# Kernel optimization log

Hardware: AMD Instinct MI355X
Metric: run time of the kernel (lower is better)

Reference implementation:

```python
import jax, jax.numpy as jnp
import numpy as np

DIM = 768
NUM_HEADS = 12
HEAD_DIM = DIM // NUM_HEADS
SCALE = HEAD_DIM ** -0.5


def setup_inputs() -> dict:
    key = jax.random.key(0)
    k1, k2, k3, k4, k5 = jax.random.split(key, 5)
    B, N = 8, 2048
    x = jax.random.normal(k1, (B, N, DIM), dtype=jnp.float32)
    mask = jax.random.randint(k2, (B, N), 0, 2, dtype=jnp.int32)
    # ensure at least one valid key per batch row to avoid all -inf softmax rows
    mask = mask.at[:, 0].set(1)
    w_qkv = jax.random.normal(k3, (DIM, 3 * DIM), dtype=jnp.float32) * (DIM ** -0.5)
    w_proj = jax.random.normal(k4, (DIM, DIM), dtype=jnp.float32) * (DIM ** -0.5)
    b_proj = jax.random.normal(k5, (DIM,), dtype=jnp.float32) * 0.02
    return {"x": x, "mask": mask, "w_qkv": w_qkv, "w_proj": w_proj, "b_proj": b_proj}


def reference(x, mask, w_qkv, w_proj, b_proj):
    B, N, C = x.shape
    qkv = (x @ w_qkv).reshape(B, N, 3, NUM_HEADS, HEAD_DIM)
    qkv = jnp.transpose(qkv, (2, 0, 3, 1, 4))  # [3, B, H, N, D]
    q, k, v = qkv[0], qkv[1], qkv[2]
    q = q * SCALE
    # fp32 upcast for scores (inputs already fp32; explicit for fidelity)
    attn = jnp.einsum('bhqd,bhkd->bhqk', q.astype(jnp.float32), k.astype(jnp.float32))
    key_mask = mask.astype(bool)[:, None, None, :]  # [B,1,1,N]
    attn = jnp.where(key_mask, attn, -jnp.inf)
    attn = jax.nn.softmax(attn, axis=-1).astype(x.dtype)
    out = jnp.einsum('bhqk,bhkd->bhqd', attn, v)  # [B,H,N,D]
    out = jnp.transpose(out, (0, 2, 1, 3)).reshape(B, N, C)
    return out @ w_proj + b_proj
```

## Files before the change

kernel.cpp:

```cpp
#include <hip/hip_runtime.h>
#include <hip/hip_bf16.h>
#include <stdint.h>

#define NHEAD 12
#define SEQ   2048
#define NB    8
#define MTOK  (NB*SEQ)
#define DIMC  768
#define QKVN  (3*DIMC)

typedef __attribute__((ext_vector_type(8))) short bf16x8;
typedef __attribute__((ext_vector_type(4))) float f32x4;
typedef __attribute__((ext_vector_type(16))) float f32x16;
typedef __attribute__((ext_vector_type(4))) unsigned short u16x4;
typedef __attribute__((ext_vector_type(4))) unsigned int u32x4;

typedef const __attribute__((address_space(1))) char glb_char;
typedef __attribute__((address_space(3))) char lds_char;

__device__ __forceinline__ unsigned short f2bf(float f) {
  union { float f; unsigned u; } v; v.f = f;
  return (unsigned short)((v.u + 0x7FFFu + ((v.u >> 16) & 1u)) >> 16);
}

__device__ __forceinline__ void gload_lds16(const void* g, void* l) {
  __builtin_amdgcn_global_load_lds((glb_char*)g, (lds_char*)l, 16, 0, 0);
}

__device__ __forceinline__ unsigned cvtpk_bf16(float lo, float hi) {
  unsigned d;
  asm("v_cvt_pk_bf16_f32 %0, %1, %2" : "=v"(d) : "v"(lo), "v"(hi));
  return d;
}

#define QSCALE 0.18033688011112042f
#define MASKBIAS -30000.0f

__global__ void __launch_bounds__(256, 8)
cvt_bf16_kernel(const float* __restrict__ in,
                unsigned short* __restrict__ out, int n4) {
  int idx = blockIdx.x * blockDim.x + threadIdx.x;
  int stride = gridDim.x * blockDim.x;
  for (int i = idx; i < n4; i += stride) {
    float4 v = ((const float4*)in)[i];
    u16x4 o;
    o.x = f2bf(v.x); o.y = f2bf(v.y); o.z = f2bf(v.z); o.w = f2bf(v.w);
    ((u16x4*)out)[i] = o;
  }
}

__global__ void __launch_bounds__(256, 4)
maskscan_kernel(const int* __restrict__ mask, int* __restrict__ posmap,
                float* __restrict__ mbias_c, int* __restrict__ nvalid) {
  __shared__ int sums[256];
  __shared__ int btot;
  const int b = blockIdx.x, t = threadIdx.x;
  const int* m = mask + b * SEQ;
  int loc[8];
  int s = 0;
  #pragma unroll
  for (int i = 0; i < 8; i++) { loc[i] = (m[t * 8 + i] != 0) ? 1 : 0; s += loc[i]; }
  sums[t] = s;
  __syncthreads();
  for (int off = 1; off < 256; off <<= 1) {
    int v = (t >= off) ? sums[t - off] : 0;
    __syncthreads();
    sums[t] += v;
    __syncthreads();
  }
  int excl = sums[t] - s;
  if (t == 255) btot = sums[255];
  __syncthreads();
  const int nv = btot;
  #pragma unroll
  for (int i = 0; i < 8; i++) {
    posmap[b * SEQ + t * 8 + i] = loc[i] ? excl : -1;
    excl += loc[i];
  }
  for (int j = t; j < SEQ; j += 256)
    mbias_c[b * SEQ + j] = (j < nv) ? 0.0f : MASKBIAS;
  if (t == 0) nvalid[b] = nv;
}

__global__ void __launch_bounds__(256, 8)
zerotail_kernel(unsigned short* __restrict__ kc, unsigned short* __restrict__ vc,
                const int* __restrict__ nvalid) {
  const int bh = blockIdx.x, t = threadIdx.x;
  const int b = bh / NHEAD;
  const int nv = nvalid[b];
  const int pad = (nv + 63) & ~63;
  const int nz = pad - nv;
  if (nz == 0) return;
  unsigned short* kcb = kc + (size_t)bh * SEQ * 64;
  unsigned short* vcb = vc + (size_t)bh * 64 * SEQ;
  for (int i = t; i < nz * 64; i += 256) {
    int r = i >> 6, d = i & 63;
    kcb[(nv + r) * 64 + d] = 0;
  }
  for (int i = t; i < 64 * nz; i += 256) {
    int d = i / nz, c = i - d * nz;
    vcb[(size_t)d * SEQ + nv + c] = 0;
  }
}

__global__ void __launch_bounds__(256, 8)
transpose_cvt_kernel(const float* __restrict__ in,
                     unsigned short* __restrict__ out,
                     int R, int C) {
  __shared__ float tile[32][33];
  int c0 = blockIdx.x * 32, r0 = blockIdx.y * 32;
  int tx = threadIdx.x & 31, ty = threadIdx.x >> 5;
  #pragma unroll
  for (int i = 0; i < 32; i += 8)
    tile[ty + i][tx] = in[(size_t)(r0 + ty + i) * C + c0 + tx];
  __syncthreads();
  #pragma unroll
  for (int i = 0; i < 32; i += 8)
    out[(size_t)(c0 + ty + i) * R + r0 + tx] = f2bf(tile[tx][ty + i]);
}

__global__ void __launch_bounds__(256, 2)
qkv_gemm_kernel(const unsigned short* __restrict__ xb,
                const unsigned short* __restrict__ wT,
                unsigned short* __restrict__ qo,
                unsigned short* __restrict__ ko,
                unsigned short* __restrict__ vto,
                const int* __restrict__ posmap) {
  __shared__ short lA[2][128 * 32];
  __shared__ short lB[2][128 * 32];
  const int t = threadIdx.x;
  const int lane = t & 63, w = t >> 6;
  const int m0 = blockIdx.x * 128;
  const int n0 = blockIdx.y * 128;
  const int wr = (w >> 1) * 64, wc = (w & 1) * 64;
  const int l15 = lane & 15, lg = lane >> 4;
  const int sr = t >> 2;
  const int sc = t & 3;

  auto STAGE = [&](int k0, int bsel) {
    #pragma unroll
    for (int i = 0; i < 2; i++) {
      int row = i * 64 + sr;
      int cb = (sc ^ ((row >> 1) & 3)) * 8;
      gload_lds16(xb + (size_t)(m0 + row) * DIMC + k0 + cb,
                  (char*)lA + bsel * 8192 + i * 4096 + w * 1024);
      gload_lds16(wT + (size_t)(n0 + row) * DIMC + k0 + cb,
                  (char*)lB + bsel * 8192 + i * 4096 + w * 1024);
    }
  };

  f32x4 acc[4][4] = {};

  STAGE(0, 0);
  asm volatile("s_waitcnt vmcnt(0)" ::: "memory");
  __builtin_amdgcn_s_barrier();

  for (int k0 = 0; k0 < DIMC; k0 += 32) {
    const int bsel = (k0 >> 5) & 1;
    if (k0 + 32 < DIMC) STAGE(k0 + 32, bsel ^ 1);
    const short* A = &lA[bsel][0];
    const short* B = &lB[bsel][0];

    bf16x8 af[4], bfr[4];
    #pragma unroll
    for (int mi = 0; mi < 4; mi++) {
      int m = wr + mi * 16 + l15;
      af[mi] = *(const bf16x8*)&A[m * 32 + ((lg ^ ((m >> 1) & 3)) << 3)];
    }
    #pragma unroll
    for (int nj = 0; nj < 4; nj++) {
      int n = wc + nj * 16 + l15;
      bfr[nj] = *(const bf16x8*)&B[n * 32 + ((lg ^ ((n >> 1) & 3)) << 3)];
    }
    __builtin_amdgcn_s_setprio(1);
    #pragma unroll
    for (int mi = 0; mi < 4; mi++)
      #pragma unroll
      for (int nj = 0; nj < 4; nj++)
        acc[mi][nj] = __builtin_amdgcn_mfma_f32_16x16x32_bf16(af[mi], bfr[nj], acc[mi][nj], 0, 0, 0);
    __builtin_amdgcn_s_setprio(0);

    if (k0 + 32 < DIMC) {
      asm volatile("s_waitcnt vmcnt(0)" ::: "memory");
      __builtin_amdgcn_s_barrier();
    }
  }

  #pragma unroll
  for (int mi = 0; mi < 4; mi++) {
    int tok0 = m0 + wr + mi * 16 + 4 * lg;
    int bb = tok0 >> 11;
    int nn0 = tok0 & 2047;
    int pm[4];
    #pragma unroll
    for (int r = 0; r < 4; r++) pm[r] = posmap[tok0 + r];
    #pragma unroll
    for (int nj = 0; nj < 4; nj++) {
      int col = n0 + wc + nj * 16 + l15;
      int which = col / DIMC;
      int ch = col - which * DIMC;
      int hh = ch >> 6, dd = ch & 63;
      size_t hb = (size_t)(bb * NHEAD + hh);
      if (which == 0) {
        size_t base = (hb * SEQ + nn0) * 64 + dd;
        #pragma unroll
        for (int r = 0; r < 4; r++)
          qo[base + (size_t)r * 64] = f2bf(acc[mi][nj][r] * QSCALE);
      } else if (which == 1) {
        #pragma unroll
        for (int r = 0; r < 4; r++)
          if (pm[r] >= 0)
            ko[(hb * SEQ + pm[r]) * 64 + dd] = f2bf(acc[mi][nj][r]);
      } else {
        #pragma unroll
        for (int r = 0; r < 4; r++)
          if (pm[r] >= 0)
            vto[(hb * 64 + dd) * SEQ + pm[r]] = f2bf(acc[mi][nj][r]);
      }
    }
  }
}

__global__ void __launch_bounds__(256, 4)
attn_kernel(const unsigned short* __restrict__ qbuf,
            const unsigned short* __restrict__ kbuf,
            const unsigned short* __restrict__ vtbuf,
            const float* __restrict__ mbias_c,
            const int* __restrict__ nvalid,
            unsigned short* __restrict__ ao) {
  __shared__ short lKV[2][8192];
  __shared__ float lmask[2][64];
  const int t = threadIdx.x, lane = t & 63, w = t >> 6;
  const int l31 = lane & 31, hi = lane >> 5;
  const int bid = blockIdx.x;
  const int qt = bid / 96;
  const int bh = bid - qt * 96;
  const int b = bh / NHEAD, h = bh - b * NHEAD;
  const int q0 = qt * 128 + w * 32;
  const unsigned short* qb = qbuf + (size_t)bh * SEQ * 64;
  const unsigned short* kb = kbuf + (size_t)bh * SEQ * 64;
  const unsigned short* vb = vtbuf + (size_t)bh * 64 * SEQ;
  const float* mb = mbias_c + b * SEQ;
  const int ntiles = (nvalid[b] + 63) >> 6;

  auto STAGE = [&](int tile, int bsel) {
    int kv0 = tile * 64;
    #pragma unroll
    for (int i = 0; i < 2; i++) {
      int c = i * 4 + w;
      gload_lds16(kb + (size_t)(kv0 + lane) * 64 + c * 8,
                  (char*)lKV + bsel * 16384 + c * 1024);
      gload_lds16(vb + (size_t)lane * SEQ + kv0 + c * 8,
                  (char*)lKV + bsel * 16384 + 8192 + c * 1024);
    }
    if (w == 0)
      __builtin_amdgcn_global_load_lds((glb_char*)(mb + tile * 64 + lane),
                                       (lds_char*)&lmask[bsel][0], 4, 0, 0);
  };

  bf16x8 qf[4];
  #pragma unroll
  for (int dblk = 0; dblk < 4; dblk++)
    qf[dblk] = *(const bf16x8*)(qb + (size_t)(q0 + l31) * 64 + dblk * 16 + hi * 8);

  f32x16 O[2] = {};
  float ls[4] = {0.f, 0.f, 0.f, 0.f};

  STAGE(0, 0);
  __syncthreads();

  for (int it = 0; it < ntiles; ++it) {
    const int bsel = it & 1;
    const short* Kb = &lKV[bsel][0];
    const short* Vb = &lKV[bsel][4096];
    if (it + 1 < ntiles) STAGE(it + 1, bsel ^ 1);

    #pragma unroll
    for (int kb2 = 0; kb2 < 2; kb2++) {
      f32x4 mb4[4];
      #pragma unroll
      for (int g = 0; g < 4; g++)
        mb4[g] = *(const f32x4*)&lmask[bsel][kb2 * 32 + g * 8 + hi * 4];
      f32x16 S;
      #pragma unroll
      for (int r = 0; r < 16; r++) S[r] = mb4[r >> 2][r & 3];

      __builtin_amdgcn_s_setprio(1);
      #pragma unroll
      for (int dblk = 0; dblk < 4; dblk++) {
        bf16x8 kf = *(const bf16x8*)&Kb[(dblk * 2 + hi) * 512 + (kb2 * 32 + l31) * 8];
        S = __builtin_amdgcn_mfma_f32_32x32x16_bf16(kf, qf[dblk], S, 0, 0, 0);
      }
      __builtin_amdgcn_s_setprio(0);

      float p[16];
      #pragma unroll
      for (int r = 0; r < 16; r++) p[r] = __builtin_amdgcn_exp2f(S[r]);
      #pragma unroll
      for (int r = 0; r < 16; r++) ls[r & 3] += p[r];

      #pragma unroll
      for (int half = 0; half < 2; half++) {
        unsigned a0 = cvtpk_bf16(p[half * 8 + 0], p[half * 8 + 1]);
        unsigned a1 = cvtpk_bf16(p[half * 8 + 2], p[half * 8 + 3]);
        unsigned a2 = cvtpk_bf16(p[half * 8 + 4], p[half * 8 + 5]);
        unsigned a3 = cvtpk_bf16(p[half * 8 + 6], p[half * 8 + 7]);
        asm("v_permlane32_swap_b32 %0, %1" : "+v"(a0), "+v"(a2));
        asm("v_permlane32_swap_b32 %0, %1" : "+v"(a1), "+v"(a3));
        union { u32x4 u; bf16x8 f; } cv;
        cv.u = (u32x4){a0, a1, a2, a3};
        __builtin_amdgcn_s_setprio(1);
        #pragma unroll
        for (int dt = 0; dt < 2; dt++) {
          bf16x8 vf = *(const bf16x8*)&Vb[(kb2 * 4 + half * 2 + hi) * 512 + (dt * 32 + l31) * 8];
          O[dt] = __builtin_amdgcn_mfma_f32_32x32x16_bf16(cv.f, vf, O[dt], 0, 0, 0);
        }
        __builtin_amdgcn_s_setprio(0);
      }
    }

    if (it + 1 < ntiles) {
      asm volatile("s_waitcnt vmcnt(0)" ::: "memory");
      __builtin_amdgcn_s_barrier();
    }
  }

  float* lrs = (float*)&lKV[0][0];
  float tot = (ls[0] + ls[1]) + (ls[2] + ls[3]);
  tot += __shfl_xor(tot, 32);
  lrs[w * 32 + l31] = tot;

  float inv[16];
  #pragma unroll
  for (int r = 0; r < 16; r++)
    inv[r] = 1.0f / lrs[w * 32 + (r & 3) + 8 * (r >> 2) + 4 * hi];

  #pragma unroll
  for (int dt = 0; dt < 2; dt++) {
    #pragma unroll
    for (int r = 0; r < 16; r++) {
      int qrow = q0 + (r & 3) + 8 * (r >> 2) + 4 * hi;
      size_t base = ((size_t)(b * SEQ + qrow)) * DIMC + h * 64 + dt * 32 + l31;
      ao[base] = __bfloat16_as_ushort(__float2bfloat16(O[dt][r] * inv[r]));
    }
  }
}

__global__ void __launch_bounds__(256, 2)
proj_gemm_kernel(const unsigned short* __restrict__ ab,
                 const unsigned short* __restrict__ wT,
                 const float* __restrict__ bias,
                 float* __restrict__ out) {
  __shared__ short lA[2][128 * 32];
  __shared__ short lB[2][128 * 32];
  const int t = threadIdx.x;
  const int lane = t & 63, w = t >> 6;
  const int m0 = blockIdx.x * 128;
  const int n0 = blockIdx.y * 128;
  const int wr = (w >> 1) * 64, wc = (w & 1) * 64;
  const int l15 = lane & 15, lg = lane >> 4;
  const int sr = t >> 2;
  const int sc = t & 3;

  auto STAGE = [&](int k0, int bsel) {
    #pragma unroll
    for (int i = 0; i < 2; i++) {
      int row = i * 64 + sr;
      int cb = (sc ^ ((row >> 1) & 3)) * 8;
      gload_lds16(ab + (size_t)(m0 + row) * DIMC + k0 + cb,
                  (char*)lA + bsel * 8192 + i * 4096 + w * 1024);
      gload_lds16(wT + (size_t)(n0 + row) * DIMC + k0 + cb,
                  (char*)lB + bsel * 8192 + i * 4096 + w * 1024);
    }
  };

  f32x4 acc[4][4] = {};

  STAGE(0, 0);
  asm volatile("s_waitcnt vmcnt(0)" ::: "memory");
  __builtin_amdgcn_s_barrier();

  for (int k0 = 0; k0 < DIMC; k0 += 32) {
    const int bsel = (k0 >> 5) & 1;
    if (k0 + 32 < DIMC) STAGE(k0 + 32, bsel ^ 1);
    const short* A = &lA[bsel][0];
    const short* B = &lB[bsel][0];

    bf16x8 af[4], bfr[4];
    #pragma unroll
    for (int mi = 0; mi < 4; mi++) {
      int m = wr + mi * 16 + l15;
      af[mi] = *(const bf16x8*)&A[m * 32 + ((lg ^ ((m >> 1) & 3)) << 3)];
    }
    #pragma unroll
    for (int nj = 0; nj < 4; nj++) {
      int n = wc + nj * 16 + l15;
      bfr[nj] = *(const bf16x8*)&B[n * 32 + ((lg ^ ((n >> 1) & 3)) << 3)];
    }
    __builtin_amdgcn_s_setprio(1);
    #pragma unroll
    for (int mi = 0; mi < 4; mi++)
      #pragma unroll
      for (int nj = 0; nj < 4; nj++)
        acc[mi][nj] = __builtin_amdgcn_mfma_f32_16x16x32_bf16(af[mi], bfr[nj], acc[mi][nj], 0, 0, 0);
    __builtin_amdgcn_s_setprio(0);

    if (k0 + 32 < DIMC) {
      asm volatile("s_waitcnt vmcnt(0)" ::: "memory");
      __builtin_amdgcn_s_barrier();
    }
  }

  #pragma unroll
  for (int mi = 0; mi < 4; mi++) {
    int row0 = m0 + wr + mi * 16 + 4 * lg;
    #pragma unroll
    for (int nj = 0; nj < 4; nj++) {
      int col = n0 + wc + nj * 16 + l15;
      float bv = bias[col];
      #pragma unroll
      for (int r = 0; r < 4; r++)
        out[(size_t)(row0 + r) * DIMC + col] = acc[mi][nj][r] + bv;
    }
  }
}

extern "C" void kernel_launch(void* const* d_in, const int* in_sizes, int n_in,
                              void* d_out, int out_size, void* d_ws, size_t ws_size,
                              hipStream_t stream) {
  const float* x      = (const float*)d_in[0];
  const int*   mask   = (const int*)d_in[1];
  const float* w_qkv  = (const float*)d_in[2];
  const float* w_proj = (const float*)d_in[3];
  const float* b_proj = (const float*)d_in[4];
  float* out = (float*)d_out;

  unsigned short* ws = (unsigned short*)d_ws;
  unsigned short* xb     = ws;
  unsigned short* wqkvT  = xb    + (size_t)MTOK * DIMC;
  unsigned short* wprojT = wqkvT + (size_t)QKVN * DIMC;
  unsigned short* qbuf   = wprojT + (size_t)DIMC * DIMC;
  unsigned short* kbuf   = qbuf  + (size_t)MTOK * DIMC;
  unsigned short* vtbuf  = kbuf  + (size_t)MTOK * DIMC;
  float*          mbias_c = (float*)(vtbuf + (size_t)MTOK * DIMC);
  int*            posmap  = (int*)(mbias_c + MTOK);
  int*            nvalid  = posmap + MTOK;
  unsigned short* aob    = xb;

  cvt_bf16_kernel<<<2048, 256, 0, stream>>>(x, xb, MTOK * DIMC / 4);
  maskscan_kernel<<<NB, 256, 0, stream>>>(mask, posmap, mbias_c, nvalid);
  transpose_cvt_kernel<<<dim3(QKVN / 32, DIMC / 32), 256, 0, stream>>>(w_qkv, wqkvT, DIMC, QKVN);
  transpose_cvt_kernel<<<dim3(DIMC / 32, DIMC / 32), 256, 0, stream>>>(w_proj, wprojT, DIMC, DIMC);
  qkv_gemm_kernel<<<dim3(128, 18), 256, 0, stream>>>(xb, wqkvT, qbuf, kbuf, vtbuf, posmap);
  zerotail_kernel<<<NB * NHEAD, 256, 0, stream>>>(kbuf, vtbuf, nvalid);
  attn_kernel<<<1536, 256, 0, stream>>>(qbuf, kbuf, vtbuf, mbias_c, nvalid, aob);
  proj_gemm_kernel<<<dim3(128, 6), 256, 0, stream>>>(aob, wprojT, b_proj, out);
}
```

Baseline: 218.9 us.

## Triple-buffer LDS staging in QKV and projection GEMMs with partial vmcnt waits

Both bf16 GEMM kernels move from a double-buffered to a triple-buffered LDS pipeline, loading two K-tiles ahead. Each iteration waits with vmcnt(4) for only the current tile's loads, so the next tile's loads stay in flight, and it uses a single barrier per iteration instead of a full drain. Launch bounds change from 2 to 3 blocks per SM. The intent is to hide global-load latency behind MFMA work, at the cost of more LDS per block and a tighter register budget.

```diff
diff --git a/kernel.cpp b/kernel.cpp
--- a/kernel.cpp
+++ b/kernel.cpp
@@ -119,15 +119,15 @@
     out[(size_t)(c0 + ty + i) * R + r0 + tx] = f2bf(tile[tx][ty + i]);
 }
 
-__global__ void __launch_bounds__(256, 2)
+__global__ void __launch_bounds__(256, 3)
 qkv_gemm_kernel(const unsigned short* __restrict__ xb,
                 const unsigned short* __restrict__ wT,
                 unsigned short* __restrict__ qo,
                 unsigned short* __restrict__ ko,
                 unsigned short* __restrict__ vto,
                 const int* __restrict__ posmap) {
-  __shared__ short lA[2][128 * 32];
-  __shared__ short lB[2][128 * 32];
+  __shared__ short lA[3][128 * 32];
+  __shared__ short lB[3][128 * 32];
   const int t = threadIdx.x;
   const int lane = t & 63, w = t >> 6;
   const int m0 = blockIdx.x * 128;
@@ -150,16 +150,22 @@
   };
 
   f32x4 acc[4][4] = {};
+  const int NT = DIMC / 32;
 
   STAGE(0, 0);
-  asm volatile("s_waitcnt vmcnt(0)" ::: "memory");
-  __builtin_amdgcn_s_barrier();
-
-  for (int k0 = 0; k0 < DIMC; k0 += 32) {
-    const int bsel = (k0 >> 5) & 1;
-    if (k0 + 32 < DIMC) STAGE(k0 + 32, bsel ^ 1);
-    const short* A = &lA[bsel][0];
-    const short* B = &lB[bsel][0];
+  STAGE(32, 1);
+
+  int cur = 0;
+  for (int kt = 0; kt < NT; ++kt) {
+    if (kt < NT - 1) asm volatile("s_waitcnt vmcnt(4)" ::: "memory");
+    else             asm volatile("s_waitcnt vmcnt(0)" ::: "memory");
+    __builtin_amdgcn_s_barrier();
+    if (kt + 2 < NT) {
+      int nb = cur + 2; if (nb >= 3) nb -= 3;
+      STAGE((kt + 2) * 32, nb);
+    }
+    const short* A = &lA[cur][0];
+    const short* B = &lB[cur][0];
 
     bf16x8 af[4], bfr[4];
     #pragma unroll
@@ -180,10 +186,7 @@
         acc[mi][nj] = __builtin_amdgcn_mfma_f32_16x16x32_bf16(af[mi], bfr[nj], acc[mi][nj], 0, 0, 0);
     __builtin_amdgcn_s_setprio(0);
 
-    if (k0 + 32 < DIMC) {
-      asm volatile("s_waitcnt vmcnt(0)" ::: "memory");
-      __builtin_amdgcn_s_barrier();
-    }
+    cur = (cur == 2) ? 0 : cur + 1;
   }
 
   #pragma unroll
@@ -346,13 +349,13 @@
   }
 }
 
-__global__ void __launch_bounds__(256, 2)
+__global__ void __launch_bounds__(256, 3)
 proj_gemm_kernel(const unsigned short* __restrict__ ab,
                  const unsigned short* __restrict__ wT,
                  const float* __restrict__ bias,
                  float* __restrict__ out) {
-  __shared__ short lA[2][128 * 32];
-  __shared__ short lB[2][128 * 32];
+  __shared__ short lA[3][128 * 32];
+  __shared__ short lB[3][128 * 32];
   const int t = threadIdx.x;
   const int lane = t & 63, w = t >> 6;
   const int m0 = blockIdx.x * 128;
@@ -375,16 +378,22 @@
   };
 
   f32x4 acc[4][4] = {};
+  const int NT = DIMC / 32;
 
   STAGE(0, 0);
-  asm volatile("s_waitcnt vmcnt(0)" ::: "memory");
-  __builtin_amdgcn_s_barrier();
-
-  for (int k0 = 0; k0 < DIMC; k0 += 32) {
-    const int bsel = (k0 >> 5) & 1;
-    if (k0 + 32 < DIMC) STAGE(k0 + 32, bsel ^ 1);
-    const short* A = &lA[bsel][0];
-    const short* B = &lB[bsel][0];
+  STAGE(32, 1);
+
+  int cur = 0;
+  for (int kt = 0; kt < NT; ++kt) {
+    if (kt < NT - 1) asm volatile("s_waitcnt vmcnt(4)" ::: "memory");
+    else             asm volatile("s_waitcnt vmcnt(0)" ::: "memory");
+    __builtin_amdgcn_s_barrier();
+    if (kt + 2 < NT) {
+      int nb = cur + 2; if (nb >= 3) nb -= 3;
+      STAGE((kt + 2) * 32, nb);
+    }
+    const short* A = &lA[cur][0];
+    const short* B = &lB[cur][0];
 
     bf16x8 af[4], bfr[4];
     #pragma unroll
@@ -405,10 +414,7 @@
         acc[mi][nj] = __builtin_amdgcn_mfma_f32_16x16x32_bf16(af[mi], bfr[nj], acc[mi][nj], 0, 0, 0);
     __builtin_amdgcn_s_setprio(0);
 
-    if (k0 + 32 < DIMC) {
-      asm volatile("s_waitcnt vmcnt(0)" ::: "memory");
-      __builtin_amdgcn_s_barrier();
-    }
+    cur = (cur == 2) ? 0 : cur + 1;
   }
 
   #pragma unroll
```

After: 215.0 us. Within noise of the previous version (-1.8%).
